# Optimization experiments

Measured on AMD Instinct MI355X. Metric: run time of the kernel, lower is better.

## Reference

```python
import jax, jax.numpy as jnp
import numpy as np

NUM_TOKENS = 16384
DIM = 4096
N_EXPERTS = 256
ROUTE_SCALE = 1.0


def setup_inputs() -> dict:
    key = jax.random.key(0)
    k_x, k_w = jax.random.split(key)
    x = jax.random.normal(k_x, (NUM_TOKENS, DIM), dtype=jnp.float32)
    # nn.init.normal_(weight, std=0.02)
    weight = 0.02 * jax.random.normal(k_w, (N_EXPERTS, DIM), dtype=jnp.float32)
    return {"x": x, "weight": weight}


def reference(x, weight):
    # Router GEMM: [T, D] @ [D, E] -> [T, E]
    scores = jnp.einsum("td,ed->te", x, weight)
    # Eval-mode token_choice path: softmax in fp32
    probs = jax.nn.softmax(scores.astype(jnp.float32), axis=-1)  # [T, E]
    indices = jnp.argmax(probs, axis=-1, keepdims=True)  # [T, 1] int
    # Hard one-hot scatter of argmax
    y_hard = jax.nn.one_hot(indices[:, 0], N_EXPERTS, dtype=probs.dtype)  # [T, E]
    # Straight-through estimator mix
    ste = jax.lax.stop_gradient(y_hard - probs) + probs
    # Gather routing weight at the selected expert
    weights = jnp.take_along_axis(ste, indices, axis=-1)  # [T, 1]
    weights = (weights * ROUTE_SCALE).astype(x.dtype)
    return weights, indices
```

## Files before the change

kernel.cpp:

```cpp
#include <hip/hip_runtime.h>
#include <stdint.h>

#define NUM_TOKENS 16384
#define DIM        4096
#define NEXP       256
#define MB         64
#define BK         64
#define APAD       72
#define NWAVES     8
#define MARGIN     2e-3f
#define CAP        16384

typedef __attribute__((ext_vector_type(4))) float   f32x4;
typedef __attribute__((ext_vector_type(8))) __bf16  bf16x8;
typedef __attribute__((ext_vector_type(8))) unsigned short u16x8;

static __device__ __forceinline__ unsigned short f32_to_bf16(float f) {
    unsigned int u = __float_as_uint(f);
    u += 0x7fffu + ((u >> 16) & 1u);
    return (unsigned short)(u >> 16);
}
static __device__ __forceinline__ float bf16_to_f32(unsigned short h) {
    return __uint_as_float(((unsigned int)h) << 16);
}

__global__ void split_weights(const float* __restrict__ w,
                              unsigned short* __restrict__ whi,
                              unsigned short* __restrict__ wlo,
                              int* __restrict__ counter) {
    if (blockIdx.x == 0 && threadIdx.x == 0) *counter = 0;
    const int n4 = NEXP * DIM / 4;
    const int stride = gridDim.x * blockDim.x;
    for (int i = blockIdx.x * blockDim.x + threadIdx.x; i < n4; i += stride) {
        float4 v = ((const float4*)w)[i];
        ushort4 h, l;
        h.x = f32_to_bf16(v.x); l.x = f32_to_bf16(v.x - bf16_to_f32(h.x));
        h.y = f32_to_bf16(v.y); l.y = f32_to_bf16(v.y - bf16_to_f32(h.y));
        h.z = f32_to_bf16(v.z); l.z = f32_to_bf16(v.z - bf16_to_f32(h.z));
        h.w = f32_to_bf16(v.w); l.w = f32_to_bf16(v.w - bf16_to_f32(h.w));
        ((ushort4*)whi)[i] = h;
        ((ushort4*)wlo)[i] = l;
    }
}

__global__ __launch_bounds__(512, 2) void gate_main(
    const float* __restrict__ x,
    const unsigned short* __restrict__ whi,
    const unsigned short* __restrict__ wlo,
    float* __restrict__ out,
    int* __restrict__ counter,
    int4* __restrict__ entries)
{
    __shared__ unsigned short lAh[MB][APAD];
    __shared__ unsigned short lAl[MB][APAD];
    __shared__ unsigned short lBh[NEXP * BK];
    __shared__ unsigned short lBl[NEXP * BK];
    __shared__ float4 cand[NWAVES][MB];

    const int tid  = threadIdx.x;
    const int wv   = tid >> 6;
    const int lane = tid & 63;
    const int tok0 = blockIdx.x * MB;

    const int ta   = tid >> 3;
    const int kseg = (tid & 7) * 8;
    const float* xrow = x + (size_t)(tok0 + ta) * DIM + kseg;

    const int esub   = lane >> 3;
    const int bk_off = ((lane & 7) ^ esub) * 8;

    const int quad = lane >> 4;
    const int col  = lane & 15;

    f32x4 acc[4][2];
    #pragma unroll
    for (int mt = 0; mt < 4; ++mt) {
        acc[mt][0] = f32x4{0.f, 0.f, 0.f, 0.f};
        acc[mt][1] = f32x4{0.f, 0.f, 0.f, 0.f};
    }

    for (int k0 = 0; k0 < DIM; k0 += BK) {
        #pragma unroll
        for (int jj = 0; jj < 4; ++jj) {
            const int e = jj * 64 + wv * 8 + esub;
            const unsigned short* gh = whi + (size_t)e * DIM + k0 + bk_off;
            const unsigned short* gl = wlo + (size_t)e * DIM + k0 + bk_off;
            unsigned short* dh = &lBh[jj * 4096 + wv * 512];
            unsigned short* dl = &lBl[jj * 4096 + wv * 512];
            __builtin_amdgcn_global_load_lds(
                (const __attribute__((address_space(1))) unsigned int*)gh,
                (__attribute__((address_space(3))) unsigned int*)dh, 16, 0, 0);
            __builtin_amdgcn_global_load_lds(
                (const __attribute__((address_space(1))) unsigned int*)gl,
                (__attribute__((address_space(3))) unsigned int*)dl, 16, 0, 0);
        }

        float4 v0 = *(const float4*)(xrow + k0);
        float4 v1 = *(const float4*)(xrow + k0 + 4);
        u16x8 vh, vl;
        #define SPLIT1(val, idx) { unsigned short _h = f32_to_bf16(val); \
            vh[idx] = _h; vl[idx] = f32_to_bf16((val) - bf16_to_f32(_h)); }
        SPLIT1(v0.x, 0) SPLIT1(v0.y, 1) SPLIT1(v0.z, 2) SPLIT1(v0.w, 3)
        SPLIT1(v1.x, 4) SPLIT1(v1.y, 5) SPLIT1(v1.z, 6) SPLIT1(v1.w, 7)
        #undef SPLIT1
        *(u16x8*)&lAh[ta][kseg] = vh;
        *(u16x8*)&lAl[ta][kseg] = vl;

        __syncthreads();

        #pragma unroll
        for (int kk = 0; kk < BK; kk += 32) {
            const int kc = kk >> 3;
            bf16x8 ah[4], al[4], bh[2], bl[2];
            #pragma unroll
            for (int mt = 0; mt < 4; ++mt) {
                ah[mt] = *(const bf16x8*)&lAh[mt * 16 + col][kk + quad * 8];
                al[mt] = *(const bf16x8*)&lAl[mt * 16 + col][kk + quad * 8];
            }
            #pragma unroll
            for (int nt = 0; nt < 2; ++nt) {
                const int e = wv * 32 + nt * 16 + col;
                const int cpos = (((kc + quad) ^ (e & 7)) * 8);
                bh[nt] = *(const bf16x8*)&lBh[e * BK + cpos];
                bl[nt] = *(const bf16x8*)&lBl[e * BK + cpos];
            }
            #pragma unroll
            for (int mt = 0; mt < 4; ++mt) {
                #pragma unroll
                for (int nt = 0; nt < 2; ++nt) {
                    acc[mt][nt] = __builtin_amdgcn_mfma_f32_16x16x32_bf16(ah[mt], bh[nt], acc[mt][nt], 0, 0, 0);
                    acc[mt][nt] = __builtin_amdgcn_mfma_f32_16x16x32_bf16(ah[mt], bl[nt], acc[mt][nt], 0, 0, 0);
                    acc[mt][nt] = __builtin_amdgcn_mfma_f32_16x16x32_bf16(al[mt], bh[nt], acc[mt][nt], 0, 0, 0);
                }
            }
        }
        __syncthreads();
    }

    #pragma unroll
    for (int mt = 0; mt < 4; ++mt) {
        #pragma unroll
        for (int r = 0; r < 4; ++r) {
            float s0 = acc[mt][0][r]; int e0 = wv * 32 + col;
            float s1 = acc[mt][1][r]; int e1 = e0 + 16;
            float t1s, t2s; int t1e, t2e;
            if (s1 > s0) { t1s = s1; t1e = e1; t2s = s0; t2e = e0; }
            else         { t1s = s0; t1e = e0; t2s = s1; t2e = e1; }
            #pragma unroll
            for (int m = 1; m <= 8; m <<= 1) {
                float o1s = __shfl_xor(t1s, m); int o1e = __shfl_xor(t1e, m);
                float o2s = __shfl_xor(t2s, m); int o2e = __shfl_xor(t2e, m);
                bool o1_top = (o1s > t1s) || (o1s == t1s && o1e < t1e);
                if (o1_top) {
                    bool keep_t1 = (t1s > o2s) || (t1s == o2s && t1e < o2e);
                    t2s = keep_t1 ? t1s : o2s; t2e = keep_t1 ? t1e : o2e;
                    t1s = o1s; t1e = o1e;
                } else {
                    bool o1_2nd = (o1s > t2s) || (o1s == t2s && o1e < t2e);
                    if (o1_2nd) { t2s = o1s; t2e = o1e; }
                }
            }
            if (col == 0) {
                int tok = mt * 16 + quad * 4 + r;
                cand[wv][tok] = make_float4(t1s, __int_as_float(t1e), t2s, __int_as_float(t2e));
            }
        }
    }
    __syncthreads();

    if (tid < MB) {
        float4 c0 = cand[0][tid];
        float t1s = c0.x; int t1e = __float_as_int(c0.y);
        float t2s = c0.z; int t2e = __float_as_int(c0.w);
        #pragma unroll
        for (int wvi = 1; wvi < NWAVES; ++wvi) {
            float4 c = cand[wvi][tid];
            float o1s = c.x; int o1e = __float_as_int(c.y);
            float o2s = c.z; int o2e = __float_as_int(c.w);
            bool o1_top = (o1s > t1s) || (o1s == t1s && o1e < t1e);
            if (o1_top) {
                bool keep_t1 = (t1s > o2s) || (t1s == o2s && t1e < o2e);
                t2s = keep_t1 ? t1s : o2s; t2e = keep_t1 ? t1e : o2e;
                t1s = o1s; t1e = o1e;
            } else {
                bool o1_2nd = (o1s > t2s) || (o1s == t2s && o1e < t2e);
                if (o1_2nd) { t2s = o1s; t2e = o1e; }
            }
        }
        const int gtok = tok0 + tid;
        out[gtok] = 1.0f;
        out[NUM_TOKENS + gtok] = (float)t1e;
        if (t1s - t2s < MARGIN) {
            int slot = atomicAdd(counter, 1);
            if (slot < CAP) entries[slot] = make_int4(gtok, t1e, t2e, 0);
        }
    }
}

__global__ void refine(const float* __restrict__ x,
                       const float* __restrict__ w,
                       const int* __restrict__ counter,
                       const int4* __restrict__ entries,
                       float* __restrict__ out) {
    const int gwave  = (blockIdx.x * blockDim.x + threadIdx.x) >> 6;
    const int lane   = threadIdx.x & 63;
    const int nwaves = (gridDim.x * blockDim.x) >> 6;
    int n = *counter; if (n > CAP) n = CAP;
    for (int i = gwave; i < n; i += nwaves) {
        int4 e = entries[i];
        const float* xr = x + (size_t)e.x * DIM;
        const float* w1 = w + (size_t)e.y * DIM;
        const float* w2 = w + (size_t)e.z * DIM;
        double d1 = 0.0, d2 = 0.0;
        for (int k = lane; k < DIM; k += 64) {
            double xv = (double)xr[k];
            d1 += xv * (double)w1[k];
            d2 += xv * (double)w2[k];
        }
        #pragma unroll
        for (int m = 32; m > 0; m >>= 1) {
            d1 += __shfl_xor(d1, m);
            d2 += __shfl_xor(d2, m);
        }
        if (lane == 0) {
            int best = (d1 > d2) ? e.y : ((d2 > d1) ? e.z : (e.y < e.z ? e.y : e.z));
            out[NUM_TOKENS + e.x] = (float)best;
        }
    }
}

extern "C" void kernel_launch(void* const* d_in, const int* in_sizes, int n_in,
                              void* d_out, int out_size, void* d_ws, size_t ws_size,
                              hipStream_t stream) {
    const float* x = (const float*)d_in[0];
    const float* w = (const float*)d_in[1];
    float* out = (float*)d_out;

    char* ws = (char*)d_ws;
    unsigned short* whi = (unsigned short*)ws;
    unsigned short* wlo = (unsigned short*)(ws + (size_t)NEXP * DIM * 2);
    int*  counter = (int*)(ws + (size_t)NEXP * DIM * 4);
    int4* entries = (int4*)(ws + (size_t)NEXP * DIM * 4 + 16);

    split_weights<<<256, 256, 0, stream>>>(w, whi, wlo, counter);
    gate_main<<<NUM_TOKENS / MB, 512, 0, stream>>>(x, whi, wlo, out, counter, entries);
    refine<<<32, 256, 0, stream>>>(x, w, counter, entries, out);
}
```

Baseline: 497.8 us.

## Use single bf16 GEMM with wider refine margin and double-buffered LDS

Replaces the three-pass split-bf16 (hi/lo) emulation of fp32 with a single bf16 MFMA pass, which cuts MFMA work and LDS traffic by about a factor of three. The top-2 margin for exact fp32 refinement widens from 2e-3 to 0.025 to cover the larger bf16 error, and the refine launch grows from 32 to 256 blocks to handle more candidates. The K loop is also double-buffered, prefetching the next weight and activation tile while computing the current one. The risk is many more tokens falling into refinement, or a case beyond the margin that flips an argmax.

```diff
diff --git a/kernel.cpp b/kernel.cpp
--- a/kernel.cpp
+++ b/kernel.cpp
@@ -8,7 +8,7 @@
 #define BK         64
 #define APAD       72
 #define NWAVES     8
-#define MARGIN     2e-3f
+#define MARGIN     0.025f
 #define CAP        16384
 
 typedef __attribute__((ext_vector_type(4))) float   f32x4;
@@ -20,41 +20,31 @@
     u += 0x7fffu + ((u >> 16) & 1u);
     return (unsigned short)(u >> 16);
 }
-static __device__ __forceinline__ float bf16_to_f32(unsigned short h) {
-    return __uint_as_float(((unsigned int)h) << 16);
-}
-
-__global__ void split_weights(const float* __restrict__ w,
-                              unsigned short* __restrict__ whi,
-                              unsigned short* __restrict__ wlo,
-                              int* __restrict__ counter) {
+
+__global__ void cvt_weights(const float* __restrict__ w,
+                            unsigned short* __restrict__ wh,
+                            int* __restrict__ counter) {
     if (blockIdx.x == 0 && threadIdx.x == 0) *counter = 0;
     const int n4 = NEXP * DIM / 4;
     const int stride = gridDim.x * blockDim.x;
     for (int i = blockIdx.x * blockDim.x + threadIdx.x; i < n4; i += stride) {
         float4 v = ((const float4*)w)[i];
-        ushort4 h, l;
-        h.x = f32_to_bf16(v.x); l.x = f32_to_bf16(v.x - bf16_to_f32(h.x));
-        h.y = f32_to_bf16(v.y); l.y = f32_to_bf16(v.y - bf16_to_f32(h.y));
-        h.z = f32_to_bf16(v.z); l.z = f32_to_bf16(v.z - bf16_to_f32(h.z));
-        h.w = f32_to_bf16(v.w); l.w = f32_to_bf16(v.w - bf16_to_f32(h.w));
-        ((ushort4*)whi)[i] = h;
-        ((ushort4*)wlo)[i] = l;
+        ushort4 h;
+        h.x = f32_to_bf16(v.x); h.y = f32_to_bf16(v.y);
+        h.z = f32_to_bf16(v.z); h.w = f32_to_bf16(v.w);
+        ((ushort4*)wh)[i] = h;
     }
 }
 
 __global__ __launch_bounds__(512, 2) void gate_main(
     const float* __restrict__ x,
-    const unsigned short* __restrict__ whi,
-    const unsigned short* __restrict__ wlo,
+    const unsigned short* __restrict__ wh,
     float* __restrict__ out,
     int* __restrict__ counter,
     int4* __restrict__ entries)
 {
-    __shared__ unsigned short lAh[MB][APAD];
-    __shared__ unsigned short lAl[MB][APAD];
-    __shared__ unsigned short lBh[NEXP * BK];
-    __shared__ unsigned short lBl[NEXP * BK];
+    __shared__ unsigned short lAh[2][MB][APAD];
+    __shared__ unsigned short lBh[2][NEXP * BK];
     __shared__ float4 cand[NWAVES][MB];
 
     const int tid  = threadIdx.x;
@@ -79,62 +69,78 @@
         acc[mt][1] = f32x4{0.f, 0.f, 0.f, 0.f};
     }
 
-    for (int k0 = 0; k0 < DIM; k0 += BK) {
+    {
         #pragma unroll
         for (int jj = 0; jj < 4; ++jj) {
             const int e = jj * 64 + wv * 8 + esub;
-            const unsigned short* gh = whi + (size_t)e * DIM + k0 + bk_off;
-            const unsigned short* gl = wlo + (size_t)e * DIM + k0 + bk_off;
-            unsigned short* dh = &lBh[jj * 4096 + wv * 512];
-            unsigned short* dl = &lBl[jj * 4096 + wv * 512];
+            const unsigned short* gh = wh + (size_t)e * DIM + bk_off;
+            unsigned short* dh = &lBh[0][jj * 4096 + wv * 512];
             __builtin_amdgcn_global_load_lds(
                 (const __attribute__((address_space(1))) unsigned int*)gh,
                 (__attribute__((address_space(3))) unsigned int*)dh, 16, 0, 0);
-            __builtin_amdgcn_global_load_lds(
-                (const __attribute__((address_space(1))) unsigned int*)gl,
-                (__attribute__((address_space(3))) unsigned int*)dl, 16, 0, 0);
-        }
-
-        float4 v0 = *(const float4*)(xrow + k0);
-        float4 v1 = *(const float4*)(xrow + k0 + 4);
-        u16x8 vh, vl;
-        #define SPLIT1(val, idx) { unsigned short _h = f32_to_bf16(val); \
-            vh[idx] = _h; vl[idx] = f32_to_bf16((val) - bf16_to_f32(_h)); }
-        SPLIT1(v0.x, 0) SPLIT1(v0.y, 1) SPLIT1(v0.z, 2) SPLIT1(v0.w, 3)
-        SPLIT1(v1.x, 4) SPLIT1(v1.y, 5) SPLIT1(v1.z, 6) SPLIT1(v1.w, 7)
-        #undef SPLIT1
-        *(u16x8*)&lAh[ta][kseg] = vh;
-        *(u16x8*)&lAl[ta][kseg] = vl;
-
+        }
+        float4 v0 = *(const float4*)(xrow);
+        float4 v1 = *(const float4*)(xrow + 4);
+        u16x8 vh;
+        vh[0] = f32_to_bf16(v0.x); vh[1] = f32_to_bf16(v0.y);
+        vh[2] = f32_to_bf16(v0.z); vh[3] = f32_to_bf16(v0.w);
+        vh[4] = f32_to_bf16(v1.x); vh[5] = f32_to_bf16(v1.y);
+        vh[6] = f32_to_bf16(v1.z); vh[7] = f32_to_bf16(v1.w);
+        *(u16x8*)&lAh[0][ta][kseg] = vh;
         __syncthreads();
+    }
+
+    int cur = 0;
+    for (int k0 = 0; k0 < DIM; k0 += BK) {
+        const int nxt = cur ^ 1;
+        const bool has_next = (k0 + BK) < DIM;
+        float4 v0, v1;
+
+        if (has_next) {
+            #pragma unroll
+            for (int jj = 0; jj < 4; ++jj) {
+                const int e = jj * 64 + wv * 8 + esub;
+                const unsigned short* gh = wh + (size_t)e * DIM + (k0 + BK) + bk_off;
+                unsigned short* dh = &lBh[nxt][jj * 4096 + wv * 512];
+                __builtin_amdgcn_global_load_lds(
+                    (const __attribute__((address_space(1))) unsigned int*)gh,
+                    (__attribute__((address_space(3))) unsigned int*)dh, 16, 0, 0);
+            }
+            v0 = *(const float4*)(xrow + k0 + BK);
+            v1 = *(const float4*)(xrow + k0 + BK + 4);
+        }
 
         #pragma unroll
         for (int kk = 0; kk < BK; kk += 32) {
             const int kc = kk >> 3;
-            bf16x8 ah[4], al[4], bh[2], bl[2];
-            #pragma unroll
-            for (int mt = 0; mt < 4; ++mt) {
-                ah[mt] = *(const bf16x8*)&lAh[mt * 16 + col][kk + quad * 8];
-                al[mt] = *(const bf16x8*)&lAl[mt * 16 + col][kk + quad * 8];
-            }
+            bf16x8 ah[4], bh[2];
+            #pragma unroll
+            for (int mt = 0; mt < 4; ++mt)
+                ah[mt] = *(const bf16x8*)&lAh[cur][mt * 16 + col][kk + quad * 8];
             #pragma unroll
             for (int nt = 0; nt < 2; ++nt) {
                 const int e = wv * 32 + nt * 16 + col;
                 const int cpos = (((kc + quad) ^ (e & 7)) * 8);
-                bh[nt] = *(const bf16x8*)&lBh[e * BK + cpos];
-                bl[nt] = *(const bf16x8*)&lBl[e * BK + cpos];
-            }
-            #pragma unroll
-            for (int mt = 0; mt < 4; ++mt) {
+                bh[nt] = *(const bf16x8*)&lBh[cur][e * BK + cpos];
+            }
+            #pragma unroll
+            for (int mt = 0; mt < 4; ++mt)
                 #pragma unroll
-                for (int nt = 0; nt < 2; ++nt) {
-                    acc[mt][nt] = __builtin_amdgcn_mfma_f32_16x16x32_bf16(ah[mt], bh[nt], acc[mt][nt], 0, 0, 0);
-                    acc[mt][nt] = __builtin_amdgcn_mfma_f32_16x16x32_bf16(ah[mt], bl[nt], acc[mt][nt], 0, 0, 0);
-                    acc[mt][nt] = __builtin_amdgcn_mfma_f32_16x16x32_bf16(al[mt], bh[nt], acc[mt][nt], 0, 0, 0);
-                }
-            }
+                for (int nt = 0; nt < 2; ++nt)
+                    acc[mt][nt] = __builtin_amdgcn_mfma_f32_16x16x32_bf16(
+                        ah[mt], bh[nt], acc[mt][nt], 0, 0, 0);
+        }
+
+        if (has_next) {
+            u16x8 vh;
+            vh[0] = f32_to_bf16(v0.x); vh[1] = f32_to_bf16(v0.y);
+            vh[2] = f32_to_bf16(v0.z); vh[3] = f32_to_bf16(v0.w);
+            vh[4] = f32_to_bf16(v1.x); vh[5] = f32_to_bf16(v1.y);
+            vh[6] = f32_to_bf16(v1.z); vh[7] = f32_to_bf16(v1.w);
+            *(u16x8*)&lAh[nxt][ta][kseg] = vh;
         }
         __syncthreads();
+        cur = nxt;
     }
 
     #pragma unroll
@@ -237,12 +243,11 @@
     float* out = (float*)d_out;
 
     char* ws = (char*)d_ws;
-    unsigned short* whi = (unsigned short*)ws;
-    unsigned short* wlo = (unsigned short*)(ws + (size_t)NEXP * DIM * 2);
-    int*  counter = (int*)(ws + (size_t)NEXP * DIM * 4);
-    int4* entries = (int4*)(ws + (size_t)NEXP * DIM * 4 + 16);
-
-    split_weights<<<256, 256, 0, stream>>>(w, whi, wlo, counter);
-    gate_main<<<NUM_TOKENS / MB, 512, 0, stream>>>(x, whi, wlo, out, counter, entries);
-    refine<<<32, 256, 0, stream>>>(x, w, counter, entries, out);
-}
+    unsigned short* wh = (unsigned short*)ws;
+    int*  counter = (int*)(ws + (size_t)NEXP * DIM * 2);
+    int4* entries = (int4*)(ws + (size_t)NEXP * DIM * 2 + 16);
+
+    cvt_weights<<<256, 256, 0, stream>>>(w, wh, counter);
+    gate_main<<<NUM_TOKENS / MB, 512, 0, stream>>>(x, wh, out, counter, entries);
+    refine<<<256, 256, 0, stream>>>(x, w, counter, entries, out);
+}
```

Result: faster. 440.4 us (-11.5%).
